# Kernel tuning notes

Measured on AMD Instinct MI355X. Metric: run time of the kernel, lower is better.

The kernel has to match this reference:

```python
import jax, jax.numpy as jnp
import numpy as np

B = 256        # graphs per batch (python loop in original, vectorized here)
N = 512        # nodes per graph
DEG = 16       # avg degree
E_PER = N * DEG
T = 64         # num_node_types
D = 128        # gnn_hidden_dim


def setup_inputs() -> dict:
    key = jax.random.key(0)
    ks = jax.random.split(key, 8)
    node_feat = jax.random.randint(ks[0], (B * N,), 0, T)
    offs = (jnp.arange(B) * N)[:, None]
    src = (jax.random.randint(ks[1], (B, E_PER), 0, N) + offs).reshape(-1)
    dst = (jax.random.randint(ks[2], (B, E_PER), 0, N) + offs).reshape(-1)
    emb_table = jax.random.normal(ks[3], (T, D), dtype=jnp.float32) * 0.02
    W1 = jax.random.normal(ks[4], (D, D), dtype=jnp.float32) * (1.0 / np.sqrt(D))
    b1 = jnp.zeros((D,), dtype=jnp.float32)
    W2 = jax.random.normal(ks[5], (D, D), dtype=jnp.float32) * (1.0 / np.sqrt(D))
    b2 = jnp.zeros((D,), dtype=jnp.float32)
    return {"node_feat": node_feat, "src": src, "dst": dst,
            "emb_table": emb_table, "W1": W1, "b1": b1, "W2": W2, "b2": b2}


def _gcn_layer(h, src, dst, out_isqrt, in_isqrt, W, b, n):
    # DGL GraphConv, norm='both': D_in^{-1/2} A D_out^{-1/2} h W + b
    m = (h * out_isqrt[:, None])[src]                      # [E, D] gather
    agg = jax.ops.segment_sum(m, dst, num_segments=n)      # [Ntot, D] scatter
    return (agg * in_isqrt[:, None]) @ W + b


def reference(node_feat, src, dst, emb_table, W1, b1, W2, b2):
    n = node_feat.shape[0]
    ones = jnp.ones(src.shape[0], dtype=emb_table.dtype)
    deg_out = jnp.clip(jax.ops.segment_sum(ones, src, num_segments=n), 1.0)
    deg_in = jnp.clip(jax.ops.segment_sum(ones, dst, num_segments=n), 1.0)
    out_isqrt = jax.lax.rsqrt(deg_out)
    in_isqrt = jax.lax.rsqrt(deg_in)

    h = emb_table[node_feat]                                # [Ntot, D]
    # layer 1 (dropout is eval-mode identity) + relu, layer 2 + relu
    h = jax.nn.relu(_gcn_layer(h, src, dst, out_isqrt, in_isqrt, W1, b1, n))
    h = jax.nn.relu(_gcn_layer(h, src, dst, out_isqrt, in_isqrt, W2, b2, n))

    # dgl.mean_nodes per graph, then mean_gnn_embeddings + stack -> [B, D]
    gid = jnp.arange(n) // N
    hg = jax.ops.segment_sum(h, gid, num_segments=B) / float(N)
    return hg
```

## Files before the change

kernel.cpp:

```cpp
#include <hip/hip_runtime.h>
#include <stdint.h>

#define GRAPHS 256
#define NPG    512
#define EPG    8192
#define NTOT   (GRAPHS*NPG)

typedef __attribute__((ext_vector_type(8))) short s16x8;
typedef __attribute__((ext_vector_type(4))) float f32x4;

__device__ __forceinline__ float bf2f(unsigned short u){
  union { unsigned int i; float f; } c; c.i = ((unsigned int)u)<<16; return c.f;
}
__device__ __forceinline__ unsigned short f2bf(float f){
  union { float f; unsigned int i; } c; c.f = f;
  unsigned int r = c.i + 0x7fffu + ((c.i>>16)&1u);
  return (unsigned short)(r>>16);
}

__global__ __launch_bounds__(512) void k_csr(const int* __restrict__ src,
      const int* __restrict__ dst, const int* __restrict__ ntype,
      const float* __restrict__ emb, const float* __restrict__ W1,
      const float* __restrict__ W2,
      unsigned int* __restrict__ sorted_g, int* __restrict__ start_g,
      float* __restrict__ out_isqrt, unsigned short* __restrict__ EW1T,
      unsigned short* __restrict__ W2F){
  __shared__ int hist[NPG], cursor[NPG], co[NPG], cs[NPG+1];
  __shared__ unsigned short ntype_sh[NPG];
  __shared__ unsigned int sorted[EPG];
  const int tid=threadIdx.x;
  if (blockIdx.x >= GRAPHS){
    const int gid = (blockIdx.x-GRAPHS)*512 + tid;
    if (gid < 8192){
      const int t = gid>>7, c = gid&127;
      float acc=0.f;
      #pragma unroll 4
      for (int k=0;k<128;k++) acc += emb[t*128+k]*W1[k*128+c];
      EW1T[c*64+t]=f2bf(acc);
    } else {
      const int i = gid - 8192;
      const int ks = i>>12, nt=(i>>9)&7, lane=(i>>3)&63, j=i&7;
      const int k = ks*32 + (lane>>4)*8 + j;
      const int n = nt*16 + (lane&15);
      W2F[i] = f2bf(W2[k*128+n]);
    }
    return;
  }
  const int b=blockIdx.x, eb=b*EPG, nb=b*NPG;
  hist[tid]=0; co[tid]=0; ntype_sh[tid]=(unsigned short)ntype[nb+tid];
  __syncthreads();
  int4 d4[4], s4[4];
  {
    const int4* dv = (const int4*)(dst+eb);
    const int4* sv = (const int4*)(src+eb);
    #pragma unroll
    for (int j=0;j<4;j++){
      d4[j]=dv[tid + j*512];
      s4[j]=sv[tid + j*512];
      atomicAdd(&hist[d4[j].x&(NPG-1)],1); atomicAdd(&hist[d4[j].y&(NPG-1)],1);
      atomicAdd(&hist[d4[j].z&(NPG-1)],1); atomicAdd(&hist[d4[j].w&(NPG-1)],1);
      atomicAdd(&co[s4[j].x&(NPG-1)],1);   atomicAdd(&co[s4[j].y&(NPG-1)],1);
      atomicAdd(&co[s4[j].z&(NPG-1)],1);   atomicAdd(&co[s4[j].w&(NPG-1)],1);
    }
  }
  __syncthreads();
  if (tid<64){
    int carry=0;
    #pragma unroll
    for (int c=0;c<8;c++){
      int sc=hist[64*c+tid];
      #pragma unroll
      for (int off=1;off<64;off<<=1){ int y=__shfl_up(sc,off); if (tid>=off) sc+=y; }
      cs[64*c+tid+1]=carry+sc;
      carry+=__shfl(sc,63);
    }
    if (tid==0) cs[0]=0;
  }
  __syncthreads();
  cursor[tid]=cs[tid];
  __syncthreads();
  #pragma unroll
  for (int j=0;j<4;j++){
    int dl, s, pos;
    dl=d4[j].x&(NPG-1); s=s4[j].x&(NPG-1);
    pos=atomicAdd(&cursor[dl],1);
    sorted[pos]=((unsigned int)dl<<15)|((unsigned int)ntype_sh[s]<<9)|(unsigned int)s;
    dl=d4[j].y&(NPG-1); s=s4[j].y&(NPG-1);
    pos=atomicAdd(&cursor[dl],1);
    sorted[pos]=((unsigned int)dl<<15)|((unsigned int)ntype_sh[s]<<9)|(unsigned int)s;
    dl=d4[j].z&(NPG-1); s=s4[j].z&(NPG-1);
    pos=atomicAdd(&cursor[dl],1);
    sorted[pos]=((unsigned int)dl<<15)|((unsigned int)ntype_sh[s]<<9)|(unsigned int)s;
    dl=d4[j].w&(NPG-1); s=s4[j].w&(NPG-1);
    pos=atomicAdd(&cursor[dl],1);
    sorted[pos]=((unsigned int)dl<<15)|((unsigned int)ntype_sh[s]<<9)|(unsigned int)s;
  }
  __syncthreads();
  for (int i=tid;i<EPG;i+=512) sorted_g[(size_t)eb+i] = sorted[i];
  if (tid==0) start_g[b*(NPG+1)+NPG]=cs[NPG];
  start_g[b*(NPG+1)+tid]=cs[tid];
  {
    int a=co[tid]; if(a<1)a=1;
    out_isqrt[nb+tid]=rsqrtf((float)a);
  }
}

#define A1_LDS 75280
__global__ __launch_bounds__(512) void k_agg1(
      const unsigned int* __restrict__ sorted_g, const int* __restrict__ start_g,
      const unsigned short* __restrict__ EW1T, const float* __restrict__ out_isqrt,
      const float* __restrict__ b1, const unsigned short* __restrict__ W2F,
      unsigned short* __restrict__ H2F){
  extern __shared__ char smem[];
  int*   Sint   = (int*)(smem);
  unsigned short* h1sh = (unsigned short*)(smem);
  float* wsc    = (float*)(smem + 69632);
  int*   wint   = (int*)  (smem + 71680);
  int*   sstart = (int*)  (smem + 73728);
  float* bsh    = (float*)(smem + 74756);
  const int bid=blockIdx.x;
  const int b    = ((bid>>4)<<3) | (bid&7);
  const int half = (bid>>3)&1;
  const int v0=half*256, nb=b*NPG, tid=threadIdx.x;
  for (int i=tid; i<(256*68)/4; i+=512) ((f32x4*)Sint)[i]=(f32x4){0.f,0.f,0.f,0.f};
  for (int i=tid; i<NPG; i+=512){
    const float w = out_isqrt[nb+i];
    wsc[i]=w;
    wint[i]=(int)(w*1048576.f);
  }
  for (int i=tid; i<257; i+=512) sstart[i]=start_g[b*(NPG+1)+v0+i];
  if (tid<128) bsh[tid]=b1[tid];
  __syncthreads();
  {
    const int beg=sstart[0], end=sstart[256];
    const unsigned int* sg = sorted_g + (size_t)b*EPG;
    for (int i=beg+tid; i<end; i+=512){
      const unsigned int ent = sg[i];
      const int dl = (int)(ent>>15) - v0;
      const int t  = (ent>>9)&63;
      atomicAdd(&Sint[dl*68 + t], wint[ent&511]);
    }
  }
  __syncthreads();
  const int wave=tid>>6, lane=tid&63, l16=lane&15, quad=lane>>4;
  f32x4 acc[2][8];
  #pragma unroll
  for (int rt=0;rt<2;rt++)
    #pragma unroll
    for (int nt=0;nt<8;nt++) acc[rt][nt]=(f32x4){0.f,0.f,0.f,0.f};
  #pragma unroll
  for (int ks=0; ks<4; ++ks){
    const int kc = (ks&1)*32 + quad*8;
    s16x8 a[2];
    #pragma unroll
    for (int rt=0;rt<2;rt++){
      const int m = (wave*2+rt)*16 + l16;
      const int* sp = &Sint[m*68 + kc];
      union { s16x8 v; unsigned short u[8]; } pk;
      #pragma unroll
      for (int j=0;j<8;j++){
        const float f = (float)sp[j] * (1.f/1048576.f);
        const unsigned short hi = f2bf(f);
        pk.u[j] = (ks<2) ? hi : f2bf(f - bf2f(hi));
      }
      a[rt]=pk.v;
    }
    #pragma unroll
    for (int nt=0;nt<8;nt++){
      s16x8 bfr=__builtin_bit_cast(s16x8,
          *(const uint4*)(EW1T + (size_t)(nt*16+l16)*64 + kc));
      #pragma unroll
      for (int rt=0;rt<2;rt++)
        acc[rt][nt]=__builtin_amdgcn_mfma_f32_16x16x32_bf16(a[rt],bfr,acc[rt][nt],0,0,0);
    }
  }
  float isq[2][4], os[2][4];
  #pragma unroll
  for (int rt=0;rt<2;rt++){
    const int mloc = (wave*2+rt)*16 + quad*4;
    #pragma unroll
    for (int r=0;r<4;r++){
      int d = sstart[mloc+r+1]-sstart[mloc+r]; if (d<1) d=1;
      isq[rt][r]=rsqrtf((float)d);
      os[rt][r]=wsc[v0+mloc+r];
    }
  }
  __syncthreads();
  #pragma unroll
  for (int rt=0;rt<2;rt++){
    const int mloc = (wave*2+rt)*16 + quad*4;
    #pragma unroll
    for (int nt=0;nt<8;nt++){
      const int col = nt*16+l16;
      const float bb = bsh[col];
      #pragma unroll
      for (int r=0;r<4;r++){
        const float v = fmaxf(acc[rt][nt][r]*isq[rt][r]+bb,0.f)*os[rt][r];
        h1sh[(mloc+r)*136 + col] = f2bf(v);
      }
    }
  }
  __syncthreads();
  f32x4 acc2[2][8];
  #pragma unroll
  for (int rt=0;rt<2;rt++)
    #pragma unroll
    for (int nt=0;nt<8;nt++) acc2[rt][nt]=(f32x4){0.f,0.f,0.f,0.f};
  #pragma unroll
  for (int ks=0; ks<4; ++ks){
    s16x8 a2[2];
    #pragma unroll
    for (int rt=0;rt<2;rt++){
      const int m = (wave*2+rt)*16 + l16;
      a2[rt]=__builtin_bit_cast(s16x8,
          *(const uint4*)(h1sh + m*136 + ks*32 + quad*8));
    }
    #pragma unroll
    for (int nt=0;nt<8;nt++){
      s16x8 bfr=__builtin_bit_cast(s16x8,
          *(const uint4*)(W2F + (size_t)(((ks*8+nt)*64)+lane)*8));
      #pragma unroll
      for (int rt=0;rt<2;rt++)
        acc2[rt][nt]=__builtin_amdgcn_mfma_f32_16x16x32_bf16(a2[rt],bfr,acc2[rt][nt],0,0,0);
    }
  }
  #pragma unroll
  for (int rt=0;rt<2;rt++){
    const int W = wave*2+rt;
    const int ks2 = half*8 + (W>>1);
    const int q2  = ((W&1)<<1) | (quad>>1);
    const int j0  = (quad&1)*4;
    #pragma unroll
    for (int nt=0;nt<8;nt++){
      ushort4 st;
      st.x=f2bf(acc2[rt][nt][0]); st.y=f2bf(acc2[rt][nt][1]);
      st.z=f2bf(acc2[rt][nt][2]); st.w=f2bf(acc2[rt][nt][3]);
      const size_t off = ((((size_t)b*16 + ks2)*8 + nt)*64 + q2*16 + l16)*8 + j0;
      *(ushort4*)(H2F + off) = st;
    }
  }
}

#define A2_LDS 67592
__global__ __launch_bounds__(512) void k_agg2(
      const unsigned int* __restrict__ sorted_g, const int* __restrict__ start_g,
      const unsigned short* __restrict__ H2F, const float* __restrict__ b2,
      float* __restrict__ partial){
  extern __shared__ char smem[];
  unsigned char* A = (unsigned char*)smem;
  unsigned int* A32 = (unsigned int*)smem;
  float* red = (float*)smem;
  int* sstart = (int*)(smem + 66560);
  float* bsh  = (float*)(smem + 67080);
  const int bid=blockIdx.x;
  const int b  = ((bid>>5)<<3) | (bid&7);
  const int dt = (bid>>3)&3;
  const int v0=dt*128, tid=threadIdx.x;
  for (int i=tid; i<66560/16; i+=512) ((uint4*)smem)[i]=(uint4){0u,0u,0u,0u};
  for (int i=tid; i<129; i+=512) sstart[i]=start_g[b*(NPG+1)+v0+i];
  if (tid<128) bsh[tid]=b2[tid];
  __syncthreads();
  {
    const int beg=sstart[0], end=sstart[128];
    const unsigned int* sg = sorted_g + (size_t)b*EPG;
    for (int i=beg+tid; i<end; i+=512){
      const unsigned int ent = sg[i];
      const int dl = (int)(ent>>15) - v0;
      const int s  = ent&511;
      atomicAdd(&A32[dl*130 + (s>>2)], 1u<<((s&3)*8));
    }
  }
  __syncthreads();
  const int wave=tid>>6, lane=tid&63, l16=lane&15, quad=lane>>4;
  const int mg=wave>>1, ng=wave&1;
  f32x4 acc[2][4];
  #pragma unroll
  for (int rt=0;rt<2;rt++)
    #pragma unroll
    for (int ct=0;ct<4;ct++) acc[rt][ct]=(f32x4){0.f,0.f,0.f,0.f};
  const uint4* bp[4];
  #pragma unroll
  for (int ct=0;ct<4;ct++)
    bp[ct] = (const uint4*)H2F + (((size_t)b*16)*8 + (ng*4+ct))*64 + lane;
  const unsigned char* Ab[2];
  #pragma unroll
  for (int rt=0;rt<2;rt++)
    Ab[rt] = A + ((mg*2+rt)*16 + l16)*520 + quad*8;
  #pragma unroll 2
  for (int ks=0; ks<16; ++ks){
    uint4 bq[4];
    #pragma unroll
    for (int ct=0;ct<4;ct++) bq[ct] = bp[ct][(size_t)ks*512];
    s16x8 afr[2];
    #pragma unroll
    for (int rt=0;rt<2;rt++){
      const uint2 aw = *(const uint2*)(Ab[rt] + ks*32);
      union { s16x8 v; unsigned short u[8]; } pk;
      #pragma unroll
      for (int j=0;j<4;j++){
        const float f0 = (float)((aw.x>>(8*j))&0xffu);
        const float f1 = (float)((aw.y>>(8*j))&0xffu);
        pk.u[j]   = (unsigned short)(__builtin_bit_cast(unsigned int, f0)>>16);
        pk.u[j+4] = (unsigned short)(__builtin_bit_cast(unsigned int, f1)>>16);
      }
      afr[rt]=pk.v;
    }
    #pragma unroll
    for (int rt=0;rt<2;rt++)
      #pragma unroll
      for (int ct=0;ct<4;ct++)
        acc[rt][ct]=__builtin_amdgcn_mfma_f32_16x16x32_bf16(afr[rt],
            __builtin_bit_cast(s16x8, bq[ct]), acc[rt][ct],0,0,0);
  }
  float p[4];
  #pragma unroll
  for (int ct=0;ct<4;ct++) p[ct]=0.f;
  #pragma unroll
  for (int rt=0;rt<2;rt++){
    const int mloc=(mg*2+rt)*16 + quad*4;
    float isq[4];
    #pragma unroll
    for (int r=0;r<4;r++){
      int d=sstart[mloc+r+1]-sstart[mloc+r]; if (d<1) d=1;
      isq[r]=rsqrtf((float)d);
    }
    #pragma unroll
    for (int ct=0;ct<4;ct++){
      const int col=ng*64 + ct*16 + l16;
      const float bb = bsh[col];
      #pragma unroll
      for (int r=0;r<4;r++)
        p[ct] += fmaxf(acc[rt][ct][r]*isq[r]+bb,0.f);
    }
  }
  #pragma unroll
  for (int ct=0;ct<4;ct++){
    p[ct] += __shfl_xor(p[ct],16);
    p[ct] += __shfl_xor(p[ct],32);
  }
  __syncthreads();
  if (quad==0){
    #pragma unroll
    for (int ct=0;ct<4;ct++) red[wave*64 + ct*16+l16]=p[ct];
  }
  __syncthreads();
  if (tid<128){
    const int col=tid, cg=col>>6, c6=col&63;
    float s=0.f;
    #pragma unroll
    for (int m2=0;m2<4;m2++) s += red[(m2*2+cg)*64 + c6];
    partial[(size_t)(b*4+dt)*128 + col]=s;
  }
}

__global__ __launch_bounds__(256) void k_final(const float* __restrict__ partial,
      float* __restrict__ out){
  const int gid = blockIdx.x*256 + threadIdx.x;
  const int b=gid>>7, c=gid&127;
  const float* p = partial + (size_t)(b*4)*128 + c;
  out[gid] = (p[0]+p[128]+p[256]+p[384])*(1.f/512.f);
}

extern "C" void kernel_launch(void* const* d_in, const int* in_sizes, int n_in,
                              void* d_out, int out_size, void* d_ws, size_t ws_size,
                              hipStream_t stream){
  const int* node_feat = (const int*)d_in[0];
  const int* src = (const int*)d_in[1];
  const int* dst = (const int*)d_in[2];
  const float* emb = (const float*)d_in[3];
  const float* W1  = (const float*)d_in[4];
  const float* b1  = (const float*)d_in[5];
  const float* W2  = (const float*)d_in[6];
  const float* b2  = (const float*)d_in[7];

  char* ws = (char*)d_ws;
  float* out_isqrt        = (float*)(ws);
  int* start_g            = (int*)(ws + 524288);
  unsigned int* sorted_g  = (unsigned int*)(ws + 1049600);
  unsigned short* EW1T    = (unsigned short*)(ws + 9438208);
  unsigned short* W2F     = (unsigned short*)(ws + 9454592);
  unsigned short* H2F     = (unsigned short*)(ws + 9487360);
  float* partial          = (float*)(ws + 43041792);

  (void)hipFuncSetAttribute(reinterpret_cast<const void*>(&k_agg1),
        hipFuncAttributeMaxDynamicSharedMemorySize, A1_LDS);
  (void)hipFuncSetAttribute(reinterpret_cast<const void*>(&k_agg2),
        hipFuncAttributeMaxDynamicSharedMemorySize, A2_LDS);

  k_csr<<<GRAPHS+48,512,0,stream>>>(src,dst,node_feat,emb,W1,W2,
        sorted_g,start_g,out_isqrt,EW1T,W2F);
  k_agg1<<<GRAPHS*2,512,A1_LDS,stream>>>(sorted_g,start_g,EW1T,out_isqrt,b1,
        W2F,H2F);
  k_agg2<<<GRAPHS*4,512,A2_LDS,stream>>>(sorted_g,start_g,H2F,b2,partial);
  k_final<<<128,256,0,stream>>>(partial,(float*)d_out);
}
```

Measured before the change: 140.9 us.

## Fold weight prep into CSR blocks, drop final kernel via atomics, retile agg2

The separate weight-preparation blocks are folded into the 256 CSR blocks, and the same blocks zero the output buffer. The final reduction kernel is removed: k_agg2 now atomically adds its scaled partial sums straight into the output. k_agg2 is retiled from 2x4 to 4x2 MFMA tiles per wave, reusing each B fragment across more rows, and uses a perm instruction to pack bf16 values. k_agg1 builds the hi/lo bf16 split in one pass with paired conversion. The change saves a kernel launch and some redundant conversions, at the cost of float atomics that make the summation order nondeterministic.

```diff
diff --git a/kernel.cpp b/kernel.cpp
--- a/kernel.cpp
+++ b/kernel.cpp
@@ -16,6 +16,9 @@
   union { float f; unsigned int i; } c; c.f = f;
   unsigned int r = c.i + 0x7fffu + ((c.i>>16)&1u);
   return (unsigned short)(r>>16);
+}
+__device__ __forceinline__ unsigned int cvt_pk_bf16(float a, float b){
+  return (unsigned int)f2bf(a) | ((unsigned int)f2bf(b)<<16);
 }
 
 __global__ __launch_bounds__(512) void k_csr(const int* __restrict__ src,
@@ -24,28 +27,11 @@
       const float* __restrict__ W2,
       unsigned int* __restrict__ sorted_g, int* __restrict__ start_g,
       float* __restrict__ out_isqrt, unsigned short* __restrict__ EW1T,
-      unsigned short* __restrict__ W2F){
+      unsigned short* __restrict__ W2F, float* __restrict__ outz){
   __shared__ int hist[NPG], cursor[NPG], co[NPG], cs[NPG+1];
   __shared__ unsigned short ntype_sh[NPG];
   __shared__ unsigned int sorted[EPG];
   const int tid=threadIdx.x;
-  if (blockIdx.x >= GRAPHS){
-    const int gid = (blockIdx.x-GRAPHS)*512 + tid;
-    if (gid < 8192){
-      const int t = gid>>7, c = gid&127;
-      float acc=0.f;
-      #pragma unroll 4
-      for (int k=0;k<128;k++) acc += emb[t*128+k]*W1[k*128+c];
-      EW1T[c*64+t]=f2bf(acc);
-    } else {
-      const int i = gid - 8192;
-      const int ks = i>>12, nt=(i>>9)&7, lane=(i>>3)&63, j=i&7;
-      const int k = ks*32 + (lane>>4)*8 + j;
-      const int n = nt*16 + (lane&15);
-      W2F[i] = f2bf(W2[k*128+n]);
-    }
-    return;
-  }
   const int b=blockIdx.x, eb=b*EPG, nb=b*NPG;
   hist[tid]=0; co[tid]=0; ntype_sh[tid]=(unsigned short)ntype[nb+tid];
   __syncthreads();
@@ -102,6 +88,22 @@
   {
     int a=co[tid]; if(a<1)a=1;
     out_isqrt[nb+tid]=rsqrtf((float)a);
+  }
+  if (tid < 32){
+    const int gid = b*32 + tid;
+    const int t = gid>>7, c = gid&127;
+    float acc=0.f;
+    #pragma unroll 4
+    for (int k=0;k<128;k++) acc += emb[t*128+k]*W1[k*128+c];
+    EW1T[c*64+t]=f2bf(acc);
+  } else if (tid >= 64 && tid < 128){
+    const int i = b*64 + (tid-64);
+    const int ks = i>>12, nt=(i>>9)&7, ln=(i>>3)&63, j=i&7;
+    const int k = ks*32 + (ln>>4)*8 + j;
+    const int n = nt*16 + (ln&15);
+    W2F[i] = f2bf(W2[k*128+n]);
+  } else if (tid >= 128 && tid < 160){
+    ((f32x4*)outz)[b*32 + (tid-128)] = (f32x4){0.f,0.f,0.f,0.f};
   }
 }
 
@@ -149,29 +151,34 @@
     #pragma unroll
     for (int nt=0;nt<8;nt++) acc[rt][nt]=(f32x4){0.f,0.f,0.f,0.f};
   #pragma unroll
-  for (int ks=0; ks<4; ++ks){
-    const int kc = (ks&1)*32 + quad*8;
-    s16x8 a[2];
+  for (int kh=0; kh<2; ++kh){
+    s16x8 fh[2], fl[2];
     #pragma unroll
     for (int rt=0;rt<2;rt++){
       const int m = (wave*2+rt)*16 + l16;
-      const int* sp = &Sint[m*68 + kc];
-      union { s16x8 v; unsigned short u[8]; } pk;
-      #pragma unroll
-      for (int j=0;j<8;j++){
-        const float f = (float)sp[j] * (1.f/1048576.f);
-        const unsigned short hi = f2bf(f);
-        pk.u[j] = (ks<2) ? hi : f2bf(f - bf2f(hi));
+      const int* sp = &Sint[m*68 + kh*32 + quad*8];
+      union { s16x8 v; unsigned int u[4]; } hv, lv;
+      #pragma unroll
+      for (int p=0;p<4;p++){
+        const float f0 = (float)sp[2*p]   * (1.f/1048576.f);
+        const float f1 = (float)sp[2*p+1] * (1.f/1048576.f);
+        const unsigned int h = cvt_pk_bf16(f0, f1);
+        hv.u[p] = h;
+        const float r0 = f0 - __builtin_bit_cast(float, h<<16);
+        const float r1 = f1 - __builtin_bit_cast(float, h & 0xffff0000u);
+        lv.u[p] = cvt_pk_bf16(r0, r1);
       }
-      a[rt]=pk.v;
-    }
+      fh[rt]=hv.v; fl[rt]=lv.v;
+    }
+    const int kc = kh*32 + quad*8;
     #pragma unroll
     for (int nt=0;nt<8;nt++){
       s16x8 bfr=__builtin_bit_cast(s16x8,
           *(const uint4*)(EW1T + (size_t)(nt*16+l16)*64 + kc));
-      #pragma unroll
-      for (int rt=0;rt<2;rt++)
-        acc[rt][nt]=__builtin_amdgcn_mfma_f32_16x16x32_bf16(a[rt],bfr,acc[rt][nt],0,0,0);
+      acc[0][nt]=__builtin_amdgcn_mfma_f32_16x16x32_bf16(fh[0],bfr,acc[0][nt],0,0,0);
+      acc[1][nt]=__builtin_amdgcn_mfma_f32_16x16x32_bf16(fh[1],bfr,acc[1][nt],0,0,0);
+      acc[0][nt]=__builtin_amdgcn_mfma_f32_16x16x32_bf16(fl[0],bfr,acc[0][nt],0,0,0);
+      acc[1][nt]=__builtin_amdgcn_mfma_f32_16x16x32_bf16(fl[1],bfr,acc[1][nt],0,0,0);
     }
   }
   float isq[2][4], os[2][4];
@@ -245,7 +252,7 @@
 __global__ __launch_bounds__(512) void k_agg2(
       const unsigned int* __restrict__ sorted_g, const int* __restrict__ start_g,
       const unsigned short* __restrict__ H2F, const float* __restrict__ b2,
-      float* __restrict__ partial){
+      float* __restrict__ out){
   extern __shared__ char smem[];
   unsigned char* A = (unsigned char*)smem;
   unsigned int* A32 = (unsigned int*)smem;
@@ -272,52 +279,58 @@
   }
   __syncthreads();
   const int wave=tid>>6, lane=tid&63, l16=lane&15, quad=lane>>4;
-  const int mg=wave>>1, ng=wave&1;
-  f32x4 acc[2][4];
-  #pragma unroll
-  for (int rt=0;rt<2;rt++)
-    #pragma unroll
-    for (int ct=0;ct<4;ct++) acc[rt][ct]=(f32x4){0.f,0.f,0.f,0.f};
-  const uint4* bp[4];
-  #pragma unroll
-  for (int ct=0;ct<4;ct++)
-    bp[ct] = (const uint4*)H2F + (((size_t)b*16)*8 + (ng*4+ct))*64 + lane;
-  const unsigned char* Ab[2];
-  #pragma unroll
-  for (int rt=0;rt<2;rt++)
-    Ab[rt] = A + ((mg*2+rt)*16 + l16)*520 + quad*8;
+  const int mg=wave>>2, ng=wave&3;
+  f32x4 acc[4][2];
+  #pragma unroll
+  for (int rt=0;rt<4;rt++)
+    #pragma unroll
+    for (int ct=0;ct<2;ct++) acc[rt][ct]=(f32x4){0.f,0.f,0.f,0.f};
+  const uint4* bp[2];
+  #pragma unroll
+  for (int ct=0;ct<2;ct++)
+    bp[ct] = (const uint4*)H2F + (((size_t)b*16)*8 + (ng*2+ct))*64 + lane;
+  const unsigned char* Ab[4];
+  #pragma unroll
+  for (int rt=0;rt<4;rt++)
+    Ab[rt] = A + ((mg*4+rt)*16 + l16)*520 + quad*8;
   #pragma unroll 2
   for (int ks=0; ks<16; ++ks){
-    uint4 bq[4];
-    #pragma unroll
-    for (int ct=0;ct<4;ct++) bq[ct] = bp[ct][(size_t)ks*512];
-    s16x8 afr[2];
-    #pragma unroll
-    for (int rt=0;rt<2;rt++){
+    const uint4 bq0 = bp[0][(size_t)ks*512];
+    const uint4 bq1 = bp[1][(size_t)ks*512];
+    #pragma unroll
+    for (int rt=0;rt<4;rt++){
       const uint2 aw = *(const uint2*)(Ab[rt] + ks*32);
-      union { s16x8 v; unsigned short u[8]; } pk;
-      #pragma unroll
-      for (int j=0;j<4;j++){
-        const float f0 = (float)((aw.x>>(8*j))&0xffu);
-        const float f1 = (float)((aw.y>>(8*j))&0xffu);
-        pk.u[j]   = (unsigned short)(__builtin_bit_cast(unsigned int, f0)>>16);
-        pk.u[j+4] = (unsigned short)(__builtin_bit_cast(unsigned int, f1)>>16);
+      union { s16x8 v; unsigned int u[4]; } pk;
+      {
+        const float g0=(float)( aw.x       &0xffu);
+        const float g1=(float)((aw.x>> 8u) &0xffu);
+        const float g2=(float)((aw.x>>16u) &0xffu);
+        const float g3=(float)( aw.x>>24u        );
+        pk.u[0]=__builtin_amdgcn_perm(__builtin_bit_cast(unsigned int,g1),
+                                      __builtin_bit_cast(unsigned int,g0),0x07060302u);
+        pk.u[1]=__builtin_amdgcn_perm(__builtin_bit_cast(unsigned int,g3),
+                                      __builtin_bit_cast(unsigned int,g2),0x07060302u);
       }
-      afr[rt]=pk.v;
-    }
-    #pragma unroll
-    for (int rt=0;rt<2;rt++)
-      #pragma unroll
-      for (int ct=0;ct<4;ct++)
-        acc[rt][ct]=__builtin_amdgcn_mfma_f32_16x16x32_bf16(afr[rt],
-            __builtin_bit_cast(s16x8, bq[ct]), acc[rt][ct],0,0,0);
-  }
-  float p[4];
-  #pragma unroll
-  for (int ct=0;ct<4;ct++) p[ct]=0.f;
-  #pragma unroll
-  for (int rt=0;rt<2;rt++){
-    const int mloc=(mg*2+rt)*16 + quad*4;
+      {
+        const float g0=(float)( aw.y       &0xffu);
+        const float g1=(float)((aw.y>> 8u) &0xffu);
+        const float g2=(float)((aw.y>>16u) &0xffu);
+        const float g3=(float)( aw.y>>24u        );
+        pk.u[2]=__builtin_amdgcn_perm(__builtin_bit_cast(unsigned int,g1),
+                                      __builtin_bit_cast(unsigned int,g0),0x07060302u);
+        pk.u[3]=__builtin_amdgcn_perm(__builtin_bit_cast(unsigned int,g3),
+                                      __builtin_bit_cast(unsigned int,g2),0x07060302u);
+      }
+      acc[rt][0]=__builtin_amdgcn_mfma_f32_16x16x32_bf16(pk.v,
+          __builtin_bit_cast(s16x8, bq0), acc[rt][0],0,0,0);
+      acc[rt][1]=__builtin_amdgcn_mfma_f32_16x16x32_bf16(pk.v,
+          __builtin_bit_cast(s16x8, bq1), acc[rt][1],0,0,0);
+    }
+  }
+  float p[2]; p[0]=0.f; p[1]=0.f;
+  #pragma unroll
+  for (int rt=0;rt<4;rt++){
+    const int mloc=(mg*4+rt)*16 + quad*4;
     float isq[4];
     #pragma unroll
     for (int r=0;r<4;r++){
@@ -325,8 +338,8 @@
       isq[r]=rsqrtf((float)d);
     }
     #pragma unroll
-    for (int ct=0;ct<4;ct++){
-      const int col=ng*64 + ct*16 + l16;
+    for (int ct=0;ct<2;ct++){
+      const int col=ng*32 + ct*16 + l16;
       const float bb = bsh[col];
       #pragma unroll
       for (int r=0;r<4;r++)
@@ -334,31 +347,21 @@
     }
   }
   #pragma unroll
-  for (int ct=0;ct<4;ct++){
+  for (int ct=0;ct<2;ct++){
     p[ct] += __shfl_xor(p[ct],16);
     p[ct] += __shfl_xor(p[ct],32);
   }
   __syncthreads();
   if (quad==0){
-    #pragma unroll
-    for (int ct=0;ct<4;ct++) red[wave*64 + ct*16+l16]=p[ct];
+    red[wave*32 + l16]      = p[0];
+    red[wave*32 + 16 + l16] = p[1];
   }
   __syncthreads();
   if (tid<128){
-    const int col=tid, cg=col>>6, c6=col&63;
-    float s=0.f;
-    #pragma unroll
-    for (int m2=0;m2<4;m2++) s += red[(m2*2+cg)*64 + c6];
-    partial[(size_t)(b*4+dt)*128 + col]=s;
-  }
-}
-
-__global__ __launch_bounds__(256) void k_final(const float* __restrict__ partial,
-      float* __restrict__ out){
-  const int gid = blockIdx.x*256 + threadIdx.x;
-  const int b=gid>>7, c=gid&127;
-  const float* p = partial + (size_t)(b*4)*128 + c;
-  out[gid] = (p[0]+p[128]+p[256]+p[384])*(1.f/512.f);
+    const int col=tid, ngc=col>>5, c5=col&31;
+    const float s = red[ngc*32 + c5] + red[(4+ngc)*32 + c5];
+    atomicAdd(out + (size_t)b*128 + col, s*(1.f/512.f));
+  }
 }
 
 extern "C" void kernel_launch(void* const* d_in, const int* in_sizes, int n_in,
@@ -380,17 +383,15 @@
   unsigned short* EW1T    = (unsigned short*)(ws + 9438208);
   unsigned short* W2F     = (unsigned short*)(ws + 9454592);
   unsigned short* H2F     = (unsigned short*)(ws + 9487360);
-  float* partial          = (float*)(ws + 43041792);
 
   (void)hipFuncSetAttribute(reinterpret_cast<const void*>(&k_agg1),
         hipFuncAttributeMaxDynamicSharedMemorySize, A1_LDS);
   (void)hipFuncSetAttribute(reinterpret_cast<const void*>(&k_agg2),
         hipFuncAttributeMaxDynamicSharedMemorySize, A2_LDS);
 
-  k_csr<<<GRAPHS+48,512,0,stream>>>(src,dst,node_feat,emb,W1,W2,
-        sorted_g,start_g,out_isqrt,EW1T,W2F);
+  k_csr<<<GRAPHS,512,0,stream>>>(src,dst,node_feat,emb,W1,W2,
+        sorted_g,start_g,out_isqrt,EW1T,W2F,(float*)d_out);
   k_agg1<<<GRAPHS*2,512,A1_LDS,stream>>>(sorted_g,start_g,EW1T,out_isqrt,b1,
         W2F,H2F);
-  k_agg2<<<GRAPHS*4,512,A2_LDS,stream>>>(sorted_g,start_g,H2F,b2,partial);
-  k_final<<<128,256,0,stream>>>(partial,(float*)d_out);
-}
+  k_agg2<<<GRAPHS*4,512,A2_LDS,stream>>>(sorted_g,start_g,H2F,b2,(float*)d_out);
+}
```

Result: no change. 143.3 us (+1.7%).
